# Kernel tuning notes

Hardware: AMD Instinct MI355X
Metric: run time of the kernel (lower is better)

The kernel has to match this reference:

```python
import jax, jax.numpy as jnp
import numpy as np

N = 100000   # n_nodes
E = 600000   # n_edges
H = 128      # hidden_dim
D1 = H // 2  # GAT hidden channels


def gat_conv(h_in, src, dst, W, a_src, a_dst, b, n):
    """Single-head PyG GATConv with default add_self_loops=True, negative_slope=0.2."""
    h = h_in @ W.T                                   # [n, out]
    sl = jnp.arange(n)
    s = jnp.concatenate([src, sl])                   # self loops appended
    d = jnp.concatenate([dst, sl])
    alpha_s = (h * a_src).sum(-1)                    # [n]
    alpha_d = (h * a_dst).sum(-1)                    # [n]
    e = jax.nn.leaky_relu(alpha_s[s] + alpha_d[d], 0.2)   # [E+n]
    m = jax.ops.segment_max(e, d, num_segments=n)    # per-dst max (stable softmax)
    w = jnp.exp(e - m[d])
    z = jax.ops.segment_sum(w, d, num_segments=n)
    attn = w / z[d]                                  # segment softmax over incoming edges
    out = jax.ops.segment_sum(attn[:, None] * h[s], d, num_segments=n)
    return out + b


def setup_inputs() -> dict:
    key = jax.random.key(0)
    ks = jax.random.split(key, 14)
    sc = 0.2
    return {
        "x": jax.random.normal(ks[0], (N, 1), jnp.float32),
        "edge_index": jax.random.randint(ks[1], (2, E), 0, N, dtype=jnp.int64),
        # GAT layer 1: 1 -> 64
        "W_gat1": jax.random.normal(ks[2], (D1, 1), jnp.float32) * sc,
        "a_src1": jax.random.normal(ks[3], (D1,), jnp.float32) * sc,
        "a_dst1": jax.random.normal(ks[4], (D1,), jnp.float32) * sc,
        "b_gat1": jnp.zeros((D1,), jnp.float32),
        # GAT layer 2: 64 -> 128
        "W_gat2": jax.random.normal(ks[5], (H, D1), jnp.float32) * sc,
        "a_src2": jax.random.normal(ks[6], (H,), jnp.float32) * sc,
        "a_dst2": jax.random.normal(ks[7], (H,), jnp.float32) * sc,
        "b_gat2": jnp.zeros((H,), jnp.float32),
        # linear1: 1 -> 128, linear2: 128 -> 128
        "W_lin1": jax.random.normal(ks[8], (H, 1), jnp.float32) * sc,
        "b_lin1": jnp.zeros((H,), jnp.float32),
        "W_lin2": jax.random.normal(ks[9], (H, H), jnp.float32) * (sc / np.sqrt(H)),
        "b_lin2": jnp.zeros((H,), jnp.float32),
    }


def reference(x, edge_index, W_gat1, a_src1, a_dst1, b_gat1,
              W_gat2, a_src2, a_dst2, b_gat2,
              W_lin1, b_lin1, W_lin2, b_lin2):
    src, dst = edge_index[0], edge_index[1]
    n = x.shape[0]
    # GAT stack (2 layers, ReLU between, none after last — PyG GAT default act)
    h = gat_conv(x, src, dst, W_gat1, a_src1, a_dst1, b_gat1, n)
    h = jax.nn.relu(h)
    h = gat_conv(h, src, dst, W_gat2, a_src2, a_dst2, b_gat2, n)   # [n, 128]
    x1 = h @ W_lin2.T + b_lin2
    x2 = x @ W_lin1.T + b_lin1
    return x2 + jax.nn.relu(x1)
```

## Files before the change

kernel.cpp:

```cpp
#include <hip/hip_runtime.h>
#include <hip/hip_fp16.h>
#include <math.h>

#define LRELU(v) ((v) > 0.f ? (v) : 0.2f * (v))
#define SLOT_STRIDE 32

using short8 = __attribute__((ext_vector_type(8))) short;
using f32x4  = __attribute__((ext_vector_type(4))) float;

__device__ __forceinline__ unsigned int f2bf(float f) {
    unsigned int u = __float_as_uint(f);
    u += 0x7fffu + ((u >> 16) & 1u);
    return u >> 16;
}

#define C_VAS 4
#define C_VAD 68
#define C_BC 132
#define C_WCT 260

__global__ void k0_precompute(const float* W1, const float* as1, const float* ad1,
                              const float* W2, const float* as2, const float* ad2,
                              const float* b2, const float* Wl2, const float* bl2,
                              float* consts, unsigned short* Whc, int* cnt, int N) {
    int b = blockIdx.x, t = threadIdx.x;
    if (b < 64) {
        float acc = 0.f;
#pragma unroll 8
        for (int j = 0; j < 128; ++j) acc += Wl2[t * 128 + j] * W2[j * 64 + b];
        consts[C_WCT + b * 128 + t] = acc;
        Whc[t * 64 + b] = (unsigned short)f2bf(acc);
    } else if (b == 64) {
        if (t < 64) {
            float vs = 0.f, vd = 0.f;
            for (int c = 0; c < 128; ++c) {
                float w = W2[c * 64 + t];
                vs += as2[c] * w;
                vd += ad2[c] * w;
            }
            consts[C_VAS + t] = vs;
            consts[C_VAD + t] = vd;
        }
        float acc = bl2[t];
        for (int j = 0; j < 128; ++j) acc += Wl2[t * 128 + j] * b2[j];
        consts[C_BC + t] = acc;
        if (t < 64) {
            float p = W1[t] * as1[t], q = W1[t] * ad1[t];
#pragma unroll
            for (int m = 1; m < 64; m <<= 1) { p += __shfl_xor(p, m); q += __shfl_xor(q, m); }
            if (t == 0) { consts[0] = p; consts[1] = q; }
        }
    } else {
        int i = (b - 65) * 128 + t;
        if (i < N) cnt[i] = 0;
    }
}

__global__ void k_fill(const int* src, const int* dst, int* cnt, int* slots, int E) {
    int e = blockIdx.x * blockDim.x + threadIdx.x;
    if (e >= E) return;
    int d = dst[e];
    int pos = atomicAdd(&cnt[d], 1);
    if (pos < SLOT_STRIDE) slots[(size_t)d * SLOT_STRIDE + pos] = src[e];
}

__global__ void kL1(const float* x, const float* consts, const int* cnt, const int* slots,
                    const float* W1, const float* b1,
                    float2* pk, float* a2d, int N) {
    int lane = threadIdx.x;
    int grp = lane >> 4, c = lane & 15;
    int i = (blockIdx.x * blockDim.y + threadIdx.y) * 4 + grp;
    if (i >= N) return;
    float cs = consts[0], cd = consts[1];
    float xi = x[i];
    float w0 = __expf(LRELU(xi * (cs + cd)));
    int n = min(cnt[i], SLOT_STRIDE);
    float w = 0.f, wxl = 0.f;
    if (c < n) {
        int s = slots[(size_t)i * SLOT_STRIDE + c];
        float xs = x[s];
        float ww = __expf(LRELU(cs * xs + cd * xi));
        w = ww; wxl = ww * xs;
    }
    if (n > 16) {
        int l2 = 16 + c;
        if (l2 < n) {
            int s = slots[(size_t)i * SLOT_STRIDE + l2];
            float xs = x[s];
            float ww = __expf(LRELU(cs * xs + cd * xi));
            w += ww; wxl += ww * xs;
        }
    }
#pragma unroll
    for (int m = 1; m < 16; m <<= 1) {
        w   += __shfl_xor(w, m);
        wxl += __shfl_xor(wxl, m);
    }
    float a1 = (w0 * xi + wxl) / (w0 + w);
    float4 W4 = *(const float4*)(W1 + 4 * c);
    float4 B4 = *(const float4*)(b1 + 4 * c);
    float h0 = fmaxf(a1 * W4.x + B4.x, 0.f);
    float h1 = fmaxf(a1 * W4.y + B4.y, 0.f);
    float h2 = fmaxf(a1 * W4.z + B4.z, 0.f);
    float h3 = fmaxf(a1 * W4.w + B4.w, 0.f);
    float4 vs = *(const float4*)(consts + C_VAS + 4 * c);
    float4 vd = *(const float4*)(consts + C_VAD + 4 * c);
    float ps = h0 * vs.x + h1 * vs.y + h2 * vs.z + h3 * vs.w;
    float pd = h0 * vd.x + h1 * vd.y + h2 * vd.z + h3 * vd.w;
#pragma unroll
    for (int m = 1; m < 16; m <<= 1) {
        ps += __shfl_xor(ps, m);
        pd += __shfl_xor(pd, m);
    }
    if (c == 0) {
        pk[i] = make_float2(a1, ps);
        a2d[i] = pd;
    }
}

#define EDGE(sidx) do {                                                       \
    int _s = (sidx);                                                          \
    float2 _p = pk[_s];                                                       \
    float _w = __expf(LRELU(_p.y + adi));                                     \
    z += _w;                                                                  \
    _Pragma("unroll")                                                         \
    for (int _j = 0; _j < 8; ++_j)                                            \
        acc[_j] += _w * fmaxf(_p.x * W1f[_j] + b1f[_j], 0.f);                 \
    } while (0)

__global__ void kL2O(const float* x, const float* consts, const int* cnt, const int* slots,
                     const float2* pk, const float* a2d, const float* W1, const float* b1,
                     const unsigned short* Whc, const float* Wl1, const float* bl1,
                     float* out, int N) {
    __shared__ unsigned short svh[64 * 72];
    int lane = threadIdx.x, wy = threadIdx.y;
    int tile = blockIdx.x * 64;
    int grp = lane >> 3, c = lane & 7;

    float W1f[8], b1f[8];
#pragma unroll
    for (int j = 0; j < 8; ++j) { W1f[j] = W1[8 * c + j]; b1f[j] = b1[8 * c + j]; }

#pragma unroll
    for (int pass = 0; pass < 2; ++pass) {
        int lr = wy * 16 + pass * 8 + grp;
        int i = tile + lr;
        if (i < N) {
            float adi = a2d[i];
            float2 pki = pk[i];
            float w0 = __expf(LRELU(pki.y + adi));
            float z = w0;
            float acc[8];
#pragma unroll
            for (int j = 0; j < 8; ++j)
                acc[j] = w0 * fmaxf(pki.x * W1f[j] + b1f[j], 0.f);
            const int4* sp4 = (const int4*)(slots + (size_t)i * SLOT_STRIDE);
            int n = min(cnt[i], SLOT_STRIDE);
            for (int b4 = 0; b4 < n; b4 += 4) {
                int4 s4 = sp4[b4 >> 2];
                int m = n - b4;
                if (m > 0) EDGE(s4.x);
                if (m > 1) EDGE(s4.y);
                if (m > 2) EDGE(s4.z);
                if (m > 3) EDGE(s4.w);
            }
            float inv = 1.f / z;
            uint4 o;
            o.x = f2bf(acc[0] * inv) | (f2bf(acc[1] * inv) << 16);
            o.y = f2bf(acc[2] * inv) | (f2bf(acc[3] * inv) << 16);
            o.z = f2bf(acc[4] * inv) | (f2bf(acc[5] * inv) << 16);
            o.w = f2bf(acc[6] * inv) | (f2bf(acc[7] * inv) << 16);
            *(uint4*)(&svh[lr * 72 + 8 * c]) = o;
        }
    }
    __syncthreads();

    int r = lane & 15, kg = lane >> 4;
    int lr = wy * 16 + r;
    int lrs = (tile + lr < N) ? lr : 0;
    short8 A0 = *(const short8*)(&svh[lrs * 72 + kg * 8]);
    short8 A1 = *(const short8*)(&svh[lrs * 72 + kg * 8 + 32]);

    f32x4 acc2[8];
#pragma unroll
    for (int ct = 0; ct < 8; ++ct) {
        const unsigned short* bp = Whc + (ct * 16 + r) * 64 + kg * 8;
        short8 B0 = *(const short8*)bp;
        short8 B1 = *(const short8*)(bp + 32);
        f32x4 cacc = {0.f, 0.f, 0.f, 0.f};
        cacc = __builtin_amdgcn_mfma_f32_16x16x32_bf16(A0, B0, cacc, 0, 0, 0);
        cacc = __builtin_amdgcn_mfma_f32_16x16x32_bf16(A1, B1, cacc, 0, 0, 0);
        acc2[ct] = cacc;
    }
    float xq[4];
#pragma unroll
    for (int q = 0; q < 4; ++q) {
        int node = tile + wy * 16 + kg * 4 + q;
        xq[q] = (node < N) ? x[node] : 0.f;
    }
#pragma unroll
    for (int ct = 0; ct < 8; ++ct) {
        int col = ct * 16 + r;
        float wl = Wl1[col], bl = bl1[col], bc = consts[C_BC + col];
#pragma unroll
        for (int q = 0; q < 4; ++q) {
            int node = tile + wy * 16 + kg * 4 + q;
            if (node < N)
                out[(size_t)node * 128 + col] = xq[q] * wl + bl + fmaxf(acc2[ct][q] + bc, 0.f);
        }
    }
}

extern "C" void kernel_launch(void* const* d_in, const int* in_sizes, int n_in,
                              void* d_out, int out_size, void* d_ws, size_t ws_size,
                              hipStream_t stream) {
    const float* x   = (const float*)d_in[0];
    const int*   ei  = (const int*)d_in[1];
    const float* W1  = (const float*)d_in[2];
    const float* as1 = (const float*)d_in[3];
    const float* ad1 = (const float*)d_in[4];
    const float* b1  = (const float*)d_in[5];
    const float* W2  = (const float*)d_in[6];
    const float* as2 = (const float*)d_in[7];
    const float* ad2 = (const float*)d_in[8];
    const float* b2  = (const float*)d_in[9];
    const float* Wl1 = (const float*)d_in[10];
    const float* bl1 = (const float*)d_in[11];
    const float* Wl2 = (const float*)d_in[12];
    const float* bl2 = (const float*)d_in[13];

    int N = in_sizes[0];
    int E = in_sizes[1] / 2;
    const int* srcp = ei;
    const int* dstp = ei + E;

    float* ws = (float*)d_ws;
    float* consts = ws;
    int*   cnt    = (int*)(ws + 8704);
    int*   slots  = cnt + N;
    float2* pk    = (float2*)(slots + (size_t)SLOT_STRIDE * N);
    float* a2d    = (float*)(pk + N);
    unsigned short* Whc = (unsigned short*)(a2d + N);

    float* outp = (float*)d_out;

    dim3 b256(256);
    dim3 bw(64, 4);

    int zb = 65 + (N + 127) / 128;
    k0_precompute<<<zb, 128, 0, stream>>>(W1, as1, ad1, W2, as2, ad2, b2, Wl2, bl2,
                                          consts, Whc, cnt, N);
    k_fill<<<(E + 255) / 256, b256, 0, stream>>>(srcp, dstp, cnt, slots, E);
    kL1<<<(N + 15) / 16, bw, 0, stream>>>(x, consts, cnt, slots, W1, b1, pk, a2d, N);
    kL2O<<<(N + 63) / 64, bw, 0, stream>>>(x, consts, cnt, slots, pk, a2d, W1, b1,
                                           Whc, Wl1, bl1, outp, N);
}
```

Measured before the change: 89.78 us.

## Shard node ranges across XCDs so fill and layer kernels stay L2-local

```diff
diff --git a/kernel.cpp b/kernel.cpp
--- a/kernel.cpp
+++ b/kernel.cpp
@@ -56,20 +56,30 @@
     }
 }
 
-__global__ void k_fill(const int* src, const int* dst, int* cnt, int* slots, int E) {
-    int e = blockIdx.x * blockDim.x + threadIdx.x;
-    if (e >= E) return;
-    int d = dst[e];
-    int pos = atomicAdd(&cnt[d], 1);
-    if (pos < SLOT_STRIDE) slots[(size_t)d * SLOT_STRIDE + pos] = src[e];
+__global__ void k_fill(const int* __restrict__ src, const int* __restrict__ dst,
+                       int* cnt, int* slots, int E, int NS, int nchunk) {
+    int shard = blockIdx.x & 7;
+    int chunk = blockIdx.x >> 3;
+    int per = (E + nchunk - 1) / nchunk;
+    int e0 = chunk * per;
+    int e1 = min(e0 + per, E);
+    int lo = shard * NS, hi = lo + NS;
+    for (int e = e0 + threadIdx.x; e < e1; e += blockDim.x) {
+        int d = dst[e];
+        if (d >= lo && d < hi) {
+            int pos = atomicAdd(&cnt[d], 1);
+            if (pos < SLOT_STRIDE) slots[(size_t)d * SLOT_STRIDE + pos] = src[e];
+        }
+    }
 }
 
 __global__ void kL1(const float* x, const float* consts, const int* cnt, const int* slots,
                     const float* W1, const float* b1,
-                    float2* pk, float* a2d, int N) {
+                    float2* pk, float* a2d, int N, int NS) {
     int lane = threadIdx.x;
     int grp = lane >> 4, c = lane & 15;
-    int i = (blockIdx.x * blockDim.y + threadIdx.y) * 4 + grp;
+    int b = blockIdx.x;
+    int i = (b & 7) * NS + (b >> 3) * 16 + threadIdx.y * 4 + grp;
     if (i >= N) return;
     float cs = consts[0], cd = consts[1];
     float xi = x[i];
@@ -131,10 +141,11 @@
 __global__ void kL2O(const float* x, const float* consts, const int* cnt, const int* slots,
                      const float2* pk, const float* a2d, const float* W1, const float* b1,
                      const unsigned short* Whc, const float* Wl1, const float* bl1,
-                     float* out, int N) {
+                     float* out, int N, int NS) {
     __shared__ unsigned short svh[64 * 72];
     int lane = threadIdx.x, wy = threadIdx.y;
-    int tile = blockIdx.x * 64;
+    int bidx = blockIdx.x;
+    int tile = (bidx & 7) * NS + (bidx >> 3) * 64;
     int grp = lane >> 3, c = lane & 7;
 
     float W1f[8], b1f[8];
@@ -234,6 +245,8 @@
     const int* srcp = ei;
     const int* dstp = ei + E;
 
+    int NS = (((N + 7) / 8) + 63) & ~63;
+
     float* ws = (float*)d_ws;
     float* consts = ws;
     int*   cnt    = (int*)(ws + 8704);
@@ -248,10 +261,11 @@
     dim3 bw(64, 4);
 
     int zb = 65 + (N + 127) / 128;
+    int nchunk = 256;
     k0_precompute<<<zb, 128, 0, stream>>>(W1, as1, ad1, W2, as2, ad2, b2, Wl2, bl2,
                                           consts, Whc, cnt, N);
-    k_fill<<<(E + 255) / 256, b256, 0, stream>>>(srcp, dstp, cnt, slots, E);
-    kL1<<<(N + 15) / 16, bw, 0, stream>>>(x, consts, cnt, slots, W1, b1, pk, a2d, N);
-    kL2O<<<(N + 63) / 64, bw, 0, stream>>>(x, consts, cnt, slots, pk, a2d, W1, b1,
-                                           Whc, Wl1, bl1, outp, N);
-}
+    k_fill<<<8 * nchunk, b256, 0, stream>>>(srcp, dstp, cnt, slots, E, NS, nchunk);
+    kL1<<<8 * (NS / 16), bw, 0, stream>>>(x, consts, cnt, slots, W1, b1, pk, a2d, N, NS);
+    kL2O<<<8 * (NS / 64), bw, 0, stream>>>(x, consts, cnt, slots, pk, a2d, W1, b1,
+                                           Whc, Wl1, bl1, outp, N, NS);
+}
```

New measurement: 87.20 us. -2.9%, faster.

## Shard edge bucketing by destination range with shared-memory counters

Applied to the files above, without the earlier changes.

```diff
diff --git a/kernel.cpp b/kernel.cpp
--- a/kernel.cpp
+++ b/kernel.cpp
@@ -3,7 +3,8 @@
 #include <math.h>
 
 #define LRELU(v) ((v) > 0.f ? (v) : 0.2f * (v))
-#define SLOT_STRIDE 32
+#define NSHARD 64
+#define CAP 16
 
 using short8 = __attribute__((ext_vector_type(8))) short;
 using f32x4  = __attribute__((ext_vector_type(4))) float;
@@ -22,7 +23,7 @@
 __global__ void k0_precompute(const float* W1, const float* as1, const float* ad1,
                               const float* W2, const float* as2, const float* ad2,
                               const float* b2, const float* Wl2, const float* bl2,
-                              float* consts, unsigned short* Whc, int* cnt, int N) {
+                              float* consts, unsigned short* Whc) {
     int b = blockIdx.x, t = threadIdx.x;
     if (b < 64) {
         float acc = 0.f;
@@ -30,7 +31,7 @@
         for (int j = 0; j < 128; ++j) acc += Wl2[t * 128 + j] * W2[j * 64 + b];
         consts[C_WCT + b * 128 + t] = acc;
         Whc[t * 64 + b] = (unsigned short)f2bf(acc);
-    } else if (b == 64) {
+    } else {
         if (t < 64) {
             float vs = 0.f, vd = 0.f;
             for (int c = 0; c < 128; ++c) {
@@ -50,22 +51,55 @@
             for (int m = 1; m < 64; m <<= 1) { p += __shfl_xor(p, m); q += __shfl_xor(q, m); }
             if (t == 0) { consts[0] = p; consts[1] = q; }
         }
-    } else {
-        int i = (b - 65) * 128 + t;
-        if (i < N) cnt[i] = 0;
-    }
-}
-
-__global__ void k_fill(const int* src, const int* dst, int* cnt, int* slots, int E) {
-    int e = blockIdx.x * blockDim.x + threadIdx.x;
-    if (e >= E) return;
-    int d = dst[e];
-    int pos = atomicAdd(&cnt[d], 1);
-    if (pos < SLOT_STRIDE) slots[(size_t)d * SLOT_STRIDE + pos] = src[e];
-}
-
-__global__ void kL1(const float* x, const float* consts, const int* cnt, const int* slots,
-                    const float* W1, const float* b1,
+    }
+}
+
+#define FILL_EDGE(dcomp, ecomp) do {                                          \
+    int _d = (dcomp) - lo;                                                    \
+    if ((unsigned)_d < (unsigned)NS2) {                                       \
+        int _p = atomicAdd(&lcnt[_d], 1);                                     \
+        if (_p < CAP)                                                         \
+            slots[(size_t)(lo + _d) * 32 + chunk * CAP + _p] = src[(ecomp)];  \
+    } } while (0)
+
+__global__ void __launch_bounds__(1024) k_fill(const int* __restrict__ src,
+                                               const int* __restrict__ dst,
+                                               int* __restrict__ cnt2,
+                                               int* __restrict__ slots,
+                                               int E, int NS2, int N) {
+    __shared__ int lcnt[1600];
+    int b = blockIdx.x;
+    int shard = b >> 1, chunk = b & 1;
+    int lo = shard * NS2;
+    int t = threadIdx.x;
+    for (int j = t; j < NS2; j += 1024) lcnt[j] = 0;
+    __syncthreads();
+    int half4 = (E / 2) & ~3;
+    int e0 = chunk ? half4 : 0;
+    int e1 = chunk ? E : half4;
+    int q0 = e0 >> 2;
+    int nq = (e1 - e0) >> 2;
+    const int4* dst4 = (const int4*)dst;
+    for (int q = t; q < nq; q += 1024) {
+        int4 d4 = dst4[q0 + q];
+        int e = e0 + q * 4;
+        FILL_EDGE(d4.x, e);
+        FILL_EDGE(d4.y, e + 1);
+        FILL_EDGE(d4.z, e + 2);
+        FILL_EDGE(d4.w, e + 3);
+    }
+    for (int e = e0 + (nq << 2) + t; e < e1; e += 1024) {
+        FILL_EDGE(dst[e], e);
+    }
+    __syncthreads();
+    for (int j = t; j < NS2; j += 1024) {
+        int i = lo + j;
+        if (i < N) cnt2[i * 2 + chunk] = lcnt[j];
+    }
+}
+
+__global__ void kL1(const float* x, const float* consts, const int2* cnt2,
+                    const int* slots, const float* W1, const float* b1,
                     float2* pk, float* a2d, int N) {
     int lane = threadIdx.x;
     int grp = lane >> 4, c = lane & 15;
@@ -74,22 +108,20 @@
     float cs = consts[0], cd = consts[1];
     float xi = x[i];
     float w0 = __expf(LRELU(xi * (cs + cd)));
-    int n = min(cnt[i], SLOT_STRIDE);
+    int2 c2 = cnt2[i];
+    int n1 = min(c2.x, CAP), n2 = min(c2.y, CAP);
     float w = 0.f, wxl = 0.f;
-    if (c < n) {
-        int s = slots[(size_t)i * SLOT_STRIDE + c];
+    if (c < n1) {
+        int s = slots[(size_t)i * 32 + c];
         float xs = x[s];
         float ww = __expf(LRELU(cs * xs + cd * xi));
         w = ww; wxl = ww * xs;
     }
-    if (n > 16) {
-        int l2 = 16 + c;
-        if (l2 < n) {
-            int s = slots[(size_t)i * SLOT_STRIDE + l2];
-            float xs = x[s];
-            float ww = __expf(LRELU(cs * xs + cd * xi));
-            w += ww; wxl += ww * xs;
-        }
+    if (c < n2) {
+        int s = slots[(size_t)i * 32 + CAP + c];
+        float xs = x[s];
+        float ww = __expf(LRELU(cs * xs + cd * xi));
+        w += ww; wxl += ww * xs;
     }
 #pragma unroll
     for (int m = 1; m < 16; m <<= 1) {
@@ -128,10 +160,10 @@
         acc[_j] += _w * fmaxf(_p.x * W1f[_j] + b1f[_j], 0.f);                 \
     } while (0)
 
-__global__ void kL2O(const float* x, const float* consts, const int* cnt, const int* slots,
-                     const float2* pk, const float* a2d, const float* W1, const float* b1,
-                     const unsigned short* Whc, const float* Wl1, const float* bl1,
-                     float* out, int N) {
+__global__ void kL2O(const float* x, const float* consts, const int2* cnt2,
+                     const int* slots, const float2* pk, const float* a2d,
+                     const float* W1, const float* b1, const unsigned short* Whc,
+                     const float* Wl1, const float* bl1, float* out, int N) {
     __shared__ unsigned short svh[64 * 72];
     int lane = threadIdx.x, wy = threadIdx.y;
     int tile = blockIdx.x * 64;
@@ -154,11 +186,21 @@
 #pragma unroll
             for (int j = 0; j < 8; ++j)
                 acc[j] = w0 * fmaxf(pki.x * W1f[j] + b1f[j], 0.f);
-            const int4* sp4 = (const int4*)(slots + (size_t)i * SLOT_STRIDE);
-            int n = min(cnt[i], SLOT_STRIDE);
-            for (int b4 = 0; b4 < n; b4 += 4) {
-                int4 s4 = sp4[b4 >> 2];
-                int m = n - b4;
+            int2 c2 = cnt2[i];
+            int n1 = min(c2.x, CAP), n2 = min(c2.y, CAP);
+            const int4* spA = (const int4*)(slots + (size_t)i * 32);
+            const int4* spB = (const int4*)(slots + (size_t)i * 32 + CAP);
+            for (int b4 = 0; b4 < n1; b4 += 4) {
+                int4 s4 = spA[b4 >> 2];
+                int m = n1 - b4;
+                if (m > 0) EDGE(s4.x);
+                if (m > 1) EDGE(s4.y);
+                if (m > 2) EDGE(s4.z);
+                if (m > 3) EDGE(s4.w);
+            }
+            for (int b4 = 0; b4 < n2; b4 += 4) {
+                int4 s4 = spB[b4 >> 2];
+                int m = n2 - b4;
                 if (m > 0) EDGE(s4.x);
                 if (m > 1) EDGE(s4.y);
                 if (m > 2) EDGE(s4.z);
@@ -234,24 +276,25 @@
     const int* srcp = ei;
     const int* dstp = ei + E;
 
+    int NS2 = (N + NSHARD - 1) / NSHARD;
+
     float* ws = (float*)d_ws;
     float* consts = ws;
-    int*   cnt    = (int*)(ws + 8704);
-    int*   slots  = cnt + N;
-    float2* pk    = (float2*)(slots + (size_t)SLOT_STRIDE * N);
+    int*   cnt2   = (int*)(ws + 8704);
+    int*   slots  = cnt2 + 2 * (size_t)N;
+    float2* pk    = (float2*)(slots + (size_t)32 * N);
     float* a2d    = (float*)(pk + N);
     unsigned short* Whc = (unsigned short*)(a2d + N);
 
     float* outp = (float*)d_out;
 
-    dim3 b256(256);
     dim3 bw(64, 4);
 
-    int zb = 65 + (N + 127) / 128;
-    k0_precompute<<<zb, 128, 0, stream>>>(W1, as1, ad1, W2, as2, ad2, b2, Wl2, bl2,
-                                          consts, Whc, cnt, N);
-    k_fill<<<(E + 255) / 256, b256, 0, stream>>>(srcp, dstp, cnt, slots, E);
-    kL1<<<(N + 15) / 16, bw, 0, stream>>>(x, consts, cnt, slots, W1, b1, pk, a2d, N);
-    kL2O<<<(N + 63) / 64, bw, 0, stream>>>(x, consts, cnt, slots, pk, a2d, W1, b1,
-                                           Whc, Wl1, bl1, outp, N);
-}
+    k0_precompute<<<65, 128, 0, stream>>>(W1, as1, ad1, W2, as2, ad2, b2, Wl2, bl2,
+                                          consts, Whc);
+    k_fill<<<2 * NSHARD, 1024, 0, stream>>>(srcp, dstp, cnt2, slots, E, NS2, N);
+    kL1<<<(N + 15) / 16, bw, 0, stream>>>(x, consts, (const int2*)cnt2, slots,
+                                          W1, b1, pk, a2d, N);
+    kL2O<<<(N + 63) / 64, bw, 0, stream>>>(x, consts, (const int2*)cnt2, slots, pk, a2d,
+                                           W1, b1, Whc, Wl1, bl1, outp, N);
+}
```

Result: slower. 141.8 us (+57.9%).

## Fuse four kernels into one cooperative persistent kernel with grid syncs

Applied to the files above, without the earlier changes.

```diff
diff --git a/kernel.cpp b/kernel.cpp
--- a/kernel.cpp
+++ b/kernel.cpp
@@ -1,9 +1,11 @@
 #include <hip/hip_runtime.h>
+#include <hip/hip_cooperative_groups.h>
 #include <hip/hip_fp16.h>
 #include <math.h>
 
+namespace cg = cooperative_groups;
+
 #define LRELU(v) ((v) > 0.f ? (v) : 0.2f * (v))
-#define SLOT_STRIDE 32
 
 using short8 = __attribute__((ext_vector_type(8))) short;
 using f32x4  = __attribute__((ext_vector_type(4))) float;
@@ -18,105 +20,6 @@
 #define C_VAD 68
 #define C_BC 132
 #define C_WCT 260
-
-__global__ void k0_precompute(const float* W1, const float* as1, const float* ad1,
-                              const float* W2, const float* as2, const float* ad2,
-                              const float* b2, const float* Wl2, const float* bl2,
-                              float* consts, unsigned short* Whc, int* cnt, int N) {
-    int b = blockIdx.x, t = threadIdx.x;
-    if (b < 64) {
-        float acc = 0.f;
-#pragma unroll 8
-        for (int j = 0; j < 128; ++j) acc += Wl2[t * 128 + j] * W2[j * 64 + b];
-        consts[C_WCT + b * 128 + t] = acc;
-        Whc[t * 64 + b] = (unsigned short)f2bf(acc);
-    } else if (b == 64) {
-        if (t < 64) {
-            float vs = 0.f, vd = 0.f;
-            for (int c = 0; c < 128; ++c) {
-                float w = W2[c * 64 + t];
-                vs += as2[c] * w;
-                vd += ad2[c] * w;
-            }
-            consts[C_VAS + t] = vs;
-            consts[C_VAD + t] = vd;
-        }
-        float acc = bl2[t];
-        for (int j = 0; j < 128; ++j) acc += Wl2[t * 128 + j] * b2[j];
-        consts[C_BC + t] = acc;
-        if (t < 64) {
-            float p = W1[t] * as1[t], q = W1[t] * ad1[t];
-#pragma unroll
-            for (int m = 1; m < 64; m <<= 1) { p += __shfl_xor(p, m); q += __shfl_xor(q, m); }
-            if (t == 0) { consts[0] = p; consts[1] = q; }
-        }
-    } else {
-        int i = (b - 65) * 128 + t;
-        if (i < N) cnt[i] = 0;
-    }
-}
-
-__global__ void k_fill(const int* src, const int* dst, int* cnt, int* slots, int E) {
-    int e = blockIdx.x * blockDim.x + threadIdx.x;
-    if (e >= E) return;
-    int d = dst[e];
-    int pos = atomicAdd(&cnt[d], 1);
-    if (pos < SLOT_STRIDE) slots[(size_t)d * SLOT_STRIDE + pos] = src[e];
-}
-
-__global__ void kL1(const float* x, const float* consts, const int* cnt, const int* slots,
-                    const float* W1, const float* b1,
-                    float2* pk, float* a2d, int N) {
-    int lane = threadIdx.x;
-    int grp = lane >> 4, c = lane & 15;
-    int i = (blockIdx.x * blockDim.y + threadIdx.y) * 4 + grp;
-    if (i >= N) return;
-    float cs = consts[0], cd = consts[1];
-    float xi = x[i];
-    float w0 = __expf(LRELU(xi * (cs + cd)));
-    int n = min(cnt[i], SLOT_STRIDE);
-    float w = 0.f, wxl = 0.f;
-    if (c < n) {
-        int s = slots[(size_t)i * SLOT_STRIDE + c];
-        float xs = x[s];
-        float ww = __expf(LRELU(cs * xs + cd * xi));
-        w = ww; wxl = ww * xs;
-    }
-    if (n > 16) {
-        int l2 = 16 + c;
-        if (l2 < n) {
-            int s = slots[(size_t)i * SLOT_STRIDE + l2];
-            float xs = x[s];
-            float ww = __expf(LRELU(cs * xs + cd * xi));
-            w += ww; wxl += ww * xs;
-        }
-    }
-#pragma unroll
-    for (int m = 1; m < 16; m <<= 1) {
-        w   += __shfl_xor(w, m);
-        wxl += __shfl_xor(wxl, m);
-    }
-    float a1 = (w0 * xi + wxl) / (w0 + w);
-    float4 W4 = *(const float4*)(W1 + 4 * c);
-    float4 B4 = *(const float4*)(b1 + 4 * c);
-    float h0 = fmaxf(a1 * W4.x + B4.x, 0.f);
-    float h1 = fmaxf(a1 * W4.y + B4.y, 0.f);
-    float h2 = fmaxf(a1 * W4.z + B4.z, 0.f);
-    float h3 = fmaxf(a1 * W4.w + B4.w, 0.f);
-    float4 vs = *(const float4*)(consts + C_VAS + 4 * c);
-    float4 vd = *(const float4*)(consts + C_VAD + 4 * c);
-    float ps = h0 * vs.x + h1 * vs.y + h2 * vs.z + h3 * vs.w;
-    float pd = h0 * vd.x + h1 * vd.y + h2 * vd.z + h3 * vd.w;
-#pragma unroll
-    for (int m = 1; m < 16; m <<= 1) {
-        ps += __shfl_xor(ps, m);
-        pd += __shfl_xor(pd, m);
-    }
-    if (c == 0) {
-        pk[i] = make_float2(a1, ps);
-        a2d[i] = pd;
-    }
-}
 
 #define EDGE(sidx) do {                                                       \
     int _s = (sidx);                                                          \
@@ -128,85 +31,197 @@
         acc[_j] += _w * fmaxf(_p.x * W1f[_j] + b1f[_j], 0.f);                 \
     } while (0)
 
-__global__ void kL2O(const float* x, const float* consts, const int* cnt, const int* slots,
-                     const float2* pk, const float* a2d, const float* W1, const float* b1,
-                     const unsigned short* Whc, const float* Wl1, const float* bl1,
-                     float* out, int N) {
+__global__ __launch_bounds__(256, 2) void k_all(
+    const float* __restrict__ x, const int* __restrict__ src, const int* __restrict__ dst,
+    const float* W1, const float* as1, const float* ad1, const float* b1,
+    const float* W2, const float* as2, const float* ad2, const float* b2,
+    const float* Wl1, const float* bl1, const float* Wl2, const float* bl2,
+    float* consts, unsigned short* Whc, int* cnt, int* slots,
+    float2* pk, float* a2d, float* out, int N, int E) {
+    cg::grid_group gg = cg::this_grid();
     __shared__ unsigned short svh[64 * 72];
     int lane = threadIdx.x, wy = threadIdx.y;
-    int tile = blockIdx.x * 64;
-    int grp = lane >> 3, c = lane & 7;
-
-    float W1f[8], b1f[8];
-#pragma unroll
-    for (int j = 0; j < 8; ++j) { W1f[j] = W1[8 * c + j]; b1f[j] = b1[8 * c + j]; }
-
-#pragma unroll
-    for (int pass = 0; pass < 2; ++pass) {
-        int lr = wy * 16 + pass * 8 + grp;
-        int i = tile + lr;
-        if (i < N) {
-            float adi = a2d[i];
-            float2 pki = pk[i];
-            float w0 = __expf(LRELU(pki.y + adi));
-            float z = w0;
-            float acc[8];
-#pragma unroll
-            for (int j = 0; j < 8; ++j)
-                acc[j] = w0 * fmaxf(pki.x * W1f[j] + b1f[j], 0.f);
-            const int4* sp4 = (const int4*)(slots + (size_t)i * SLOT_STRIDE);
-            int n = min(cnt[i], SLOT_STRIDE);
-            for (int b4 = 0; b4 < n; b4 += 4) {
-                int4 s4 = sp4[b4 >> 2];
-                int m = n - b4;
-                if (m > 0) EDGE(s4.x);
-                if (m > 1) EDGE(s4.y);
-                if (m > 2) EDGE(s4.z);
-                if (m > 3) EDGE(s4.w);
-            }
-            float inv = 1.f / z;
-            uint4 o;
-            o.x = f2bf(acc[0] * inv) | (f2bf(acc[1] * inv) << 16);
-            o.y = f2bf(acc[2] * inv) | (f2bf(acc[3] * inv) << 16);
-            o.z = f2bf(acc[4] * inv) | (f2bf(acc[5] * inv) << 16);
-            o.w = f2bf(acc[6] * inv) | (f2bf(acc[7] * inv) << 16);
-            *(uint4*)(&svh[lr * 72 + 8 * c]) = o;
-        }
-    }
-    __syncthreads();
-
-    int r = lane & 15, kg = lane >> 4;
-    int lr = wy * 16 + r;
-    int lrs = (tile + lr < N) ? lr : 0;
-    short8 A0 = *(const short8*)(&svh[lrs * 72 + kg * 8]);
-    short8 A1 = *(const short8*)(&svh[lrs * 72 + kg * 8 + 32]);
-
-    f32x4 acc2[8];
-#pragma unroll
-    for (int ct = 0; ct < 8; ++ct) {
-        const unsigned short* bp = Whc + (ct * 16 + r) * 64 + kg * 8;
-        short8 B0 = *(const short8*)bp;
-        short8 B1 = *(const short8*)(bp + 32);
-        f32x4 cacc = {0.f, 0.f, 0.f, 0.f};
-        cacc = __builtin_amdgcn_mfma_f32_16x16x32_bf16(A0, B0, cacc, 0, 0, 0);
-        cacc = __builtin_amdgcn_mfma_f32_16x16x32_bf16(A1, B1, cacc, 0, 0, 0);
-        acc2[ct] = cacc;
-    }
-    float xq[4];
-#pragma unroll
-    for (int q = 0; q < 4; ++q) {
-        int node = tile + wy * 16 + kg * 4 + q;
-        xq[q] = (node < N) ? x[node] : 0.f;
-    }
-#pragma unroll
-    for (int ct = 0; ct < 8; ++ct) {
-        int col = ct * 16 + r;
-        float wl = Wl1[col], bl = bl1[col], bc = consts[C_BC + col];
-#pragma unroll
-        for (int q = 0; q < 4; ++q) {
-            int node = tile + wy * 16 + kg * 4 + q;
-            if (node < N)
-                out[(size_t)node * 128 + col] = xq[q] * wl + bl + fmaxf(acc2[ct][q] + bc, 0.f);
+    int flatt = wy * 64 + lane;
+    int bid = blockIdx.x, G = gridDim.x;
+
+    for (int i = bid * 256 + flatt; i < N; i += G * 256) cnt[i] = 0;
+    if (bid < 64) {
+        int t = flatt;
+        if (t < 128) {
+            float acc = 0.f;
+#pragma unroll 8
+            for (int j = 0; j < 128; ++j) acc += Wl2[t * 128 + j] * W2[j * 64 + bid];
+            consts[C_WCT + bid * 128 + t] = acc;
+            Whc[t * 64 + bid] = (unsigned short)f2bf(acc);
+        }
+    } else if (bid == 64) {
+        int t = flatt;
+        if (t < 128) {
+            if (t < 64) {
+                float vs = 0.f, vd = 0.f;
+                for (int c = 0; c < 128; ++c) {
+                    float w = W2[c * 64 + t];
+                    vs += as2[c] * w;
+                    vd += ad2[c] * w;
+                }
+                consts[C_VAS + t] = vs;
+                consts[C_VAD + t] = vd;
+            }
+            float acc = bl2[t];
+            for (int j = 0; j < 128; ++j) acc += Wl2[t * 128 + j] * b2[j];
+            consts[C_BC + t] = acc;
+            if (t < 64) {
+                float p = W1[t] * as1[t], q = W1[t] * ad1[t];
+#pragma unroll
+                for (int m = 1; m < 64; m <<= 1) {
+                    p += __shfl_xor(p, m);
+                    q += __shfl_xor(q, m);
+                }
+                if (t == 0) { consts[0] = p; consts[1] = q; }
+            }
+        }
+    }
+    gg.sync();
+
+    for (int e = bid * 256 + flatt; e < E; e += G * 256) {
+        int d = dst[e];
+        int pos = atomicAdd(&cnt[d], 1);
+        if (pos < 32) slots[(size_t)d * 32 + pos] = src[e];
+    }
+    gg.sync();
+
+    {
+        int grp = lane >> 4, c = lane & 15;
+        float cs = consts[0], cd = consts[1];
+        float4 W4 = *(const float4*)(W1 + 4 * c);
+        float4 B4 = *(const float4*)(b1 + 4 * c);
+        float4 vs = *(const float4*)(consts + C_VAS + 4 * c);
+        float4 vd = *(const float4*)(consts + C_VAD + 4 * c);
+        int nu = (N + 3) >> 2;
+        for (int u = bid * 4 + wy; u < nu; u += G * 4) {
+            int i = u * 4 + grp;
+            if (i < N) {
+                float xi = x[i];
+                float w0 = __expf(LRELU(xi * (cs + cd)));
+                int n = min(cnt[i], 32);
+                float w = 0.f, wxl = 0.f;
+                if (c < n) {
+                    int s = slots[(size_t)i * 32 + c];
+                    float xs = x[s];
+                    float ww = __expf(LRELU(cs * xs + cd * xi));
+                    w = ww; wxl = ww * xs;
+                }
+                if (n > 16) {
+                    int l2 = 16 + c;
+                    if (l2 < n) {
+                        int s = slots[(size_t)i * 32 + l2];
+                        float xs = x[s];
+                        float ww = __expf(LRELU(cs * xs + cd * xi));
+                        w += ww; wxl += ww * xs;
+                    }
+                }
+#pragma unroll
+                for (int m = 1; m < 16; m <<= 1) {
+                    w   += __shfl_xor(w, m);
+                    wxl += __shfl_xor(wxl, m);
+                }
+                float a1 = (w0 * xi + wxl) / (w0 + w);
+                float h0 = fmaxf(a1 * W4.x + B4.x, 0.f);
+                float h1 = fmaxf(a1 * W4.y + B4.y, 0.f);
+                float h2 = fmaxf(a1 * W4.z + B4.z, 0.f);
+                float h3 = fmaxf(a1 * W4.w + B4.w, 0.f);
+                float ps = h0 * vs.x + h1 * vs.y + h2 * vs.z + h3 * vs.w;
+                float pd = h0 * vd.x + h1 * vd.y + h2 * vd.z + h3 * vd.w;
+#pragma unroll
+                for (int m = 1; m < 16; m <<= 1) {
+                    ps += __shfl_xor(ps, m);
+                    pd += __shfl_xor(pd, m);
+                }
+                if (c == 0) {
+                    pk[i] = make_float2(a1, ps);
+                    a2d[i] = pd;
+                }
+            }
+        }
+    }
+    gg.sync();
+
+    {
+        int grp8 = lane >> 3, c = lane & 7;
+        float W1f[8], b1f[8];
+#pragma unroll
+        for (int j = 0; j < 8; ++j) { W1f[j] = W1[8 * c + j]; b1f[j] = b1[8 * c + j]; }
+        int r = lane & 15, kg = lane >> 4;
+        int ntile = (N + 63) >> 6;
+        for (int ti = bid; ti < ntile; ti += G) {
+            int tile = ti * 64;
+#pragma unroll
+            for (int pass = 0; pass < 2; ++pass) {
+                int lr = wy * 16 + pass * 8 + grp8;
+                int i = tile + lr;
+                if (i < N) {
+                    float adi = a2d[i];
+                    float2 pki = pk[i];
+                    float w0 = __expf(LRELU(pki.y + adi));
+                    float z = w0;
+                    float acc[8];
+#pragma unroll
+                    for (int j = 0; j < 8; ++j)
+                        acc[j] = w0 * fmaxf(pki.x * W1f[j] + b1f[j], 0.f);
+                    const int4* sp4 = (const int4*)(slots + (size_t)i * 32);
+                    int n = min(cnt[i], 32);
+                    for (int b4 = 0; b4 < n; b4 += 4) {
+                        int4 s4 = sp4[b4 >> 2];
+                        int m = n - b4;
+                        if (m > 0) EDGE(s4.x);
+                        if (m > 1) EDGE(s4.y);
+                        if (m > 2) EDGE(s4.z);
+                        if (m > 3) EDGE(s4.w);
+                    }
+                    float inv = 1.f / z;
+                    uint4 o;
+                    o.x = f2bf(acc[0] * inv) | (f2bf(acc[1] * inv) << 16);
+                    o.y = f2bf(acc[2] * inv) | (f2bf(acc[3] * inv) << 16);
+                    o.z = f2bf(acc[4] * inv) | (f2bf(acc[5] * inv) << 16);
+                    o.w = f2bf(acc[6] * inv) | (f2bf(acc[7] * inv) << 16);
+                    *(uint4*)(&svh[lr * 72 + 8 * c]) = o;
+                }
+            }
+            __syncthreads();
+            int lr = wy * 16 + r;
+            int lrs = (tile + lr < N) ? lr : 0;
+            short8 A0 = *(const short8*)(&svh[lrs * 72 + kg * 8]);
+            short8 A1 = *(const short8*)(&svh[lrs * 72 + kg * 8 + 32]);
+            f32x4 acc2[8];
+#pragma unroll
+            for (int ct = 0; ct < 8; ++ct) {
+                const unsigned short* bp = Whc + (ct * 16 + r) * 64 + kg * 8;
+                short8 B0 = *(const short8*)bp;
+                short8 B1 = *(const short8*)(bp + 32);
+                f32x4 cacc = {0.f, 0.f, 0.f, 0.f};
+                cacc = __builtin_amdgcn_mfma_f32_16x16x32_bf16(A0, B0, cacc, 0, 0, 0);
+                cacc = __builtin_amdgcn_mfma_f32_16x16x32_bf16(A1, B1, cacc, 0, 0, 0);
+                acc2[ct] = cacc;
+            }
+            float xq[4];
+#pragma unroll
+            for (int q = 0; q < 4; ++q) {
+                int node = tile + wy * 16 + kg * 4 + q;
+                xq[q] = (node < N) ? x[node] : 0.f;
+            }
+#pragma unroll
+            for (int ct = 0; ct < 8; ++ct) {
+                int col = ct * 16 + r;
+                float wl = Wl1[col], bl = bl1[col], bc = consts[C_BC + col];
+#pragma unroll
+                for (int q = 0; q < 4; ++q) {
+                    int node = tile + wy * 16 + kg * 4 + q;
+                    if (node < N)
+                        out[(size_t)node * 128 + col] =
+                            xq[q] * wl + bl + fmaxf(acc2[ct][q] + bc, 0.f);
+                }
+            }
+            __syncthreads();
         }
     }
 }
@@ -238,20 +253,20 @@
     float* consts = ws;
     int*   cnt    = (int*)(ws + 8704);
     int*   slots  = cnt + N;
-    float2* pk    = (float2*)(slots + (size_t)SLOT_STRIDE * N);
+    float2* pk    = (float2*)(slots + (size_t)32 * N);
     float* a2d    = (float*)(pk + N);
     unsigned short* Whc = (unsigned short*)(a2d + N);
 
     float* outp = (float*)d_out;
 
-    dim3 b256(256);
-    dim3 bw(64, 4);
-
-    int zb = 65 + (N + 127) / 128;
-    k0_precompute<<<zb, 128, 0, stream>>>(W1, as1, ad1, W2, as2, ad2, b2, Wl2, bl2,
-                                          consts, Whc, cnt, N);
-    k_fill<<<(E + 255) / 256, b256, 0, stream>>>(srcp, dstp, cnt, slots, E);
-    kL1<<<(N + 15) / 16, bw, 0, stream>>>(x, consts, cnt, slots, W1, b1, pk, a2d, N);
-    kL2O<<<(N + 63) / 64, bw, 0, stream>>>(x, consts, cnt, slots, pk, a2d, W1, b1,
-                                           Whc, Wl1, bl1, outp, N);
+    void* args[] = {
+        (void*)&x, (void*)&srcp, (void*)&dstp,
+        (void*)&W1, (void*)&as1, (void*)&ad1, (void*)&b1,
+        (void*)&W2, (void*)&as2, (void*)&ad2, (void*)&b2,
+        (void*)&Wl1, (void*)&bl1, (void*)&Wl2, (void*)&bl2,
+        (void*)&consts, (void*)&Whc, (void*)&cnt, (void*)&slots,
+        (void*)&pk, (void*)&a2d, (void*)&outp, (void*)&N, (void*)&E,
+    };
+    hipLaunchCooperativeKernel((const void*)k_all, dim3(512), dim3(64, 4),
+                               args, 0, stream);
 }
```

Result: slower. 315.4 us (+251.3%).
